# Performance work log

Measured on AMD Instinct MI355X. Metric: run time of the kernel, lower is better.

The kernel has to match this reference:

```python
import jax, jax.numpy as jnp
import numpy as np
from functools import partial

L, B, D_IN, D_MODEL, D_OUT, D_STATE = 2048, 8, 128, 256, 32, 16
D_INNER, DT_RANK, K_CONV = 2 * D_MODEL, D_MODEL // 16, 4
LOG2PI = float(np.log(2.0 * np.pi))


def setup_inputs() -> dict:
    key = jax.random.key(0)
    ks = jax.random.split(key, 16)
    sc = 0.02
    inp = {
        "s": jax.random.normal(ks[0], (L, B, D_IN), jnp.float32),
        "a": jax.random.normal(ks[1], (L, B, D_OUT), jnp.float32),
        # embedding linear
        "W_emb": jax.random.normal(ks[2], (D_IN, D_MODEL), jnp.float32) * sc,
        "b_emb": jnp.zeros((D_MODEL,), jnp.float32),
        # mamba block params
        "norm_w": jnp.ones((D_MODEL,), jnp.float32),
        "W_in": jax.random.normal(ks[3], (D_MODEL, 2 * D_INNER), jnp.float32) * sc,
        "conv_w": jax.random.normal(ks[4], (D_INNER, 1, K_CONV), jnp.float32) * sc,
        "conv_b": jnp.zeros((D_INNER,), jnp.float32),
        "W_x": jax.random.normal(ks[5], (D_INNER, DT_RANK + 2 * D_STATE), jnp.float32) * sc,
        "W_dt": jax.random.normal(ks[6], (DT_RANK, D_INNER), jnp.float32) * sc,
        "b_dt": jnp.full((D_INNER,), -2.0, jnp.float32),  # softplus(-2) ~ small init dt
        "A_log": jnp.broadcast_to(jnp.log(jnp.arange(1, D_STATE + 1, dtype=jnp.float32)), (D_INNER, D_STATE)).copy(),
        "D": jnp.ones((D_INNER,), jnp.float32),
        "W_out": jax.random.normal(ks[7], (D_INNER, D_MODEL), jnp.float32) * sc,
        # action head + log_std
        "W_head": jax.random.normal(ks[8], (D_MODEL, D_OUT), jnp.float32) * sc,
        "b_head": jnp.zeros((D_OUT,), jnp.float32),
        "log_std": jnp.zeros((D_OUT,), jnp.float32),
    }
    return inp


def _rmsnorm(x, w, eps=1e-5):
    return x * jax.lax.rsqrt(jnp.mean(x * x, axis=-1, keepdims=True) + eps) * w


def _silu(x):
    return x * jax.nn.sigmoid(x)


def _mamba_block(x, norm_w, W_in, conv_w, conv_b, W_x, W_dt, b_dt, A_log, D, W_out):
    # x: (B, L, d_model)
    resid = x
    xn = _rmsnorm(x, norm_w)
    xz = xn @ W_in                                  # (B, L, 2*d_inner)
    xp, z = jnp.split(xz, 2, axis=-1)
    # causal depthwise conv over time
    xc = jax.lax.conv_general_dilated(
        xp.transpose(0, 2, 1), conv_w, window_strides=(1,),
        padding=[(K_CONV - 1, 0)], feature_group_count=D_INNER,
        dimension_numbers=("NCH", "OIH", "NCH"))
    xp = _silu((xc + conv_b[None, :, None]).transpose(0, 2, 1))  # (B, L, d_inner)
    # input-dependent SSM params
    x_dbl = xp @ W_x                                # (B, L, dt_rank + 2*d_state)
    dt, Bm, Cm = jnp.split(x_dbl, [DT_RANK, DT_RANK + D_STATE], axis=-1)
    dt = jax.nn.softplus(dt @ W_dt + b_dt)          # (B, L, d_inner)
    A = -jnp.exp(A_log)                             # (d_inner, d_state)

    def step(h, t):
        dt_t, B_t, C_t, x_t = t                     # (B,d_i) (B,d_s) (B,d_s) (B,d_i)
        dA = jnp.exp(dt_t[..., None] * A)           # (B, d_inner, d_state)
        dBx = (dt_t * x_t)[..., None] * B_t[:, None, :]
        h = dA * h + dBx
        y = jnp.einsum("bds,bs->bd", h, C_t)
        return h, y

    h0 = jnp.zeros((x.shape[0], D_INNER, D_STATE), x.dtype)
    tm = lambda u: jnp.moveaxis(u, 1, 0)            # time-major
    _, ys = jax.lax.scan(step, h0, (tm(dt), tm(Bm), tm(Cm), tm(xp)))
    y = jnp.moveaxis(ys, 0, 1) + xp * D             # (B, L, d_inner)
    y = y * _silu(z)
    return y @ W_out + resid


def reference(s, a, W_emb, b_emb, norm_w, W_in, conv_w, conv_b, W_x, W_dt, b_dt,
              A_log, D, W_out, W_head, b_head, log_std):
    x = s @ W_emb + b_emb                           # (L, B, d_model)
    x = x.transpose(1, 0, 2)                        # (B, L, d_model)
    x = _mamba_block(x, norm_w, W_in, conv_w, conv_b, W_x, W_dt, b_dt, A_log, D, W_out)
    x = x.transpose(1, 0, 2)                        # (L, B, d_model)
    mu = x @ W_head + b_head                        # (L, B, d_out)
    # Normal(mu, exp(log_std)).log_prob(a).sum(-1)
    z = (a - mu) * jnp.exp(-log_std)
    logp = -0.5 * z * z - log_std - 0.5 * LOG2PI
    return logp.sum(axis=-1)                        # (L, B)
```

## Files before the change

kernel.cpp:

```cpp
#include <hip/hip_runtime.h>

typedef unsigned short u16;
typedef short bf16x8 __attribute__((ext_vector_type(8)));
typedef float floatx4 __attribute__((ext_vector_type(4)));

#define LSEQ 2048
#define BB 8
#define NTOK (LSEQ*BB)
#define DMODEL 256
#define DINNER 512
#define NSEG 128
#define SEGLEN 16

__device__ __forceinline__ float siluf(float x){ return x / (1.f + __expf(-x)); }
__device__ __forceinline__ float b2f(u16 x){ return __uint_as_float(((unsigned)x) << 16); }
__device__ __forceinline__ u16 f2b(float f){
  unsigned u = __float_as_uint(f);
  unsigned r = (u + 0x7fffu + ((u >> 16) & 1u)) >> 16;
  return (u16)r;
}

__global__ __launch_bounds__(256) void prep_k(
    const float* __restrict__ s, const float* __restrict__ Wemb,
    const float* __restrict__ Win, const float* __restrict__ Wout,
    const float* __restrict__ Wx, const float* __restrict__ Wdt,
    const float* __restrict__ Wh,
    u16* __restrict__ sb, u16* __restrict__ WTe, u16* __restrict__ WTi,
    u16* __restrict__ WTo, u16* __restrict__ WxT, u16* __restrict__ WdtTp,
    u16* __restrict__ WhT)
{
  int g = blockIdx.x, tid = threadIdx.x;
  if (g < 2048) {
    int i = (g*256 + tid)*4;
    float4 v = *(const float4*)&s[i];
    ushort4 o; o.x=f2b(v.x); o.y=f2b(v.y); o.z=f2b(v.z); o.w=f2b(v.w);
    *(ushort4*)&sb[i] = o;
  } else if (g < 2176) {
    int idx = (g-2048)*256 + tid; int n = idx >> 7, k = idx & 127;
    WTe[idx] = f2b(Wemb[(size_t)k*256 + n]);
  } else if (g < 3200) {
    int idx = (g-2176)*256 + tid; int n = idx >> 8, k = idx & 255;
    WTi[idx] = f2b(Win[(size_t)k*1024 + n]);
  } else if (g < 3712) {
    int idx = (g-3200)*256 + tid; int n = idx >> 9, k = idx & 511;
    WTo[idx] = f2b(Wout[(size_t)k*256 + n]);
  } else if (g < 3808) {
    int idx = (g-3712)*256 + tid; int n = idx >> 9, k = idx & 511;
    WxT[idx] = f2b(Wx[(size_t)k*48 + n]);
  } else if (g < 3872) {
    int idx = (g-3808)*256 + tid; int c = idx >> 5, r = idx & 31;
    WdtTp[idx] = (r < 16) ? f2b(Wdt[(size_t)r*512 + c]) : (u16)0;
  } else {
    int idx = (g-3872)*256 + tid; int j = idx >> 8, k = idx & 255;
    WhT[idx] = f2b(Wh[(size_t)k*32 + j]);
  }
}

template<int K, int OUTB>
__global__ __launch_bounds__(256) void gemm_mfma(
    const u16* __restrict__ Ab, const u16* __restrict__ WT,
    const float* __restrict__ bias, void* __restrict__ Cv, int N)
{
  __shared__ u16 SH[128*136];
  u16* As = SH;
  u16* Bs = SH + 128*40;
  const int tid = threadIdx.x;
  const int wave = tid >> 6, lane = tid & 63;
  const int quad = lane >> 4, l16 = lane & 15;
  const int bm0 = blockIdx.x*128, bn0 = blockIdx.y*128;
  const int wm = (wave & 1)*64, wn = (wave >> 1)*64;
  const int srow = tid >> 2, sch = (tid & 3)*8;
  floatx4 acc[4][4];
  #pragma unroll
  for (int r = 0; r < 4; ++r)
    #pragma unroll
    for (int c = 0; c < 4; ++c) acc[r][c] = (floatx4){0.f,0.f,0.f,0.f};

  for (int k0 = 0; k0 < K; k0 += 32) {
    #pragma unroll
    for (int p = 0; p < 2; ++p) {
      int row = srow + p*64;
      *(uint4*)&As[row*40 + sch] = *(const uint4*)&Ab[(size_t)(bm0+row)*K + k0 + sch];
      *(uint4*)&Bs[row*40 + sch] = *(const uint4*)&WT[(size_t)(bn0+row)*K + k0 + sch];
    }
    __syncthreads();
    bf16x8 af[4], bf[4];
    #pragma unroll
    for (int r = 0; r < 4; ++r) af[r] = *(const bf16x8*)&As[(wm + r*16 + l16)*40 + quad*8];
    #pragma unroll
    for (int c = 0; c < 4; ++c) bf[c] = *(const bf16x8*)&Bs[(wn + c*16 + l16)*40 + quad*8];
    #pragma unroll
    for (int r = 0; r < 4; ++r)
      #pragma unroll
      for (int c = 0; c < 4; ++c)
        acc[r][c] = __builtin_amdgcn_mfma_f32_16x16x32_bf16(af[r], bf[c], acc[r][c], 0, 0, 0);
    __syncthreads();
  }

  if (OUTB) {
    u16* Cs = SH;
    #pragma unroll
    for (int c = 0; c < 4; ++c) {
      int nl = wn + c*16 + l16;
      float bv = bias ? bias[bn0 + nl] : 0.f;
      #pragma unroll
      for (int r = 0; r < 4; ++r)
        #pragma unroll
        for (int reg = 0; reg < 4; ++reg) {
          int ml = wm + r*16 + quad*4 + reg;
          Cs[ml*136 + nl] = f2b(acc[r][c][reg] + bv);
        }
    }
    __syncthreads();
    #pragma unroll
    for (int p = 0; p < 8; ++p) {
      int row = p*16 + (tid >> 4);
      int col = (tid & 15)*8;
      uint4 v = *(const uint4*)&Cs[row*136 + col];
      *(uint4*)&((u16*)Cv)[(size_t)(bm0+row)*N + bn0 + col] = v;
    }
  } else {
    float* Cf = (float*)SH;
    #pragma unroll
    for (int half = 0; half < 2; ++half) {
      if ((wave & 1) == half) {
        #pragma unroll
        for (int c = 0; c < 4; ++c) {
          int nl = wn + c*16 + l16;
          float bv = bias ? bias[bn0 + nl] : 0.f;
          #pragma unroll
          for (int r = 0; r < 4; ++r)
            #pragma unroll
            for (int reg = 0; reg < 4; ++reg) {
              int ml = r*16 + quad*4 + reg;
              Cf[ml*132 + nl] = acc[r][c][reg] + bv;
            }
        }
      }
      __syncthreads();
      #pragma unroll
      for (int p = 0; p < 8; ++p) {
        int row = p*8 + (tid >> 5);
        int col = (tid & 31)*4;
        float4 v = *(const float4*)&Cf[row*132 + col];
        *(float4*)&((float*)Cv)[(size_t)(bm0 + half*64 + row)*N + bn0 + col] = v;
      }
      __syncthreads();
    }
  }
}

__global__ __launch_bounds__(256) void rmsnorm_k(const float* __restrict__ X,
    const float* __restrict__ w, u16* __restrict__ XNb)
{
  int n = blockIdx.x*4 + (threadIdx.x >> 6);
  int lane = threadIdx.x & 63;
  const float4 x = *(const float4*)&X[(size_t)n*DMODEL + lane*4];
  float ss = x.x*x.x + x.y*x.y + x.z*x.z + x.w*x.w;
  #pragma unroll
  for (int m = 1; m < 64; m <<= 1) ss += __shfl_xor(ss, m);
  float r = rsqrtf(ss * (1.f/DMODEL) + 1e-5f);
  ushort4 o;
  o.x = f2b(x.x * r * w[lane*4+0]);
  o.y = f2b(x.y * r * w[lane*4+1]);
  o.z = f2b(x.z * r * w[lane*4+2]);
  o.w = f2b(x.w * r * w[lane*4+3]);
  *(ushort4*)&XNb[(size_t)n*DMODEL + lane*4] = o;
}

__global__ __launch_bounds__(256) void conv_silu_k(const u16* __restrict__ XZb,
    const float* __restrict__ cw, const float* __restrict__ cb,
    u16* __restrict__ XPb)
{
  int g = blockIdx.x*256 + threadIdx.x;
  int c4 = (g & 127) << 2;
  int n = g >> 7;
  int l = n >> 3;
  float w[4][4];
  #pragma unroll
  for (int i = 0; i < 4; ++i)
    #pragma unroll
    for (int k = 0; k < 4; ++k) w[i][k] = cw[(c4+i)*4 + k];
  float acc[4];
  #pragma unroll
  for (int i = 0; i < 4; ++i) acc[i] = cb[c4+i];
  #pragma unroll
  for (int k = 0; k < 4; ++k) {
    int lp = l - 3 + k;
    if (lp >= 0) {
      const ushort4 xv = *(const ushort4*)&XZb[(size_t)(n - BB*(3-k))*1024 + c4];
      acc[0] = fmaf(w[0][k], b2f(xv.x), acc[0]);
      acc[1] = fmaf(w[1][k], b2f(xv.y), acc[1]);
      acc[2] = fmaf(w[2][k], b2f(xv.z), acc[2]);
      acc[3] = fmaf(w[3][k], b2f(xv.w), acc[3]);
    }
  }
  ushort4 ob;
  ob.x = f2b(siluf(acc[0])); ob.y = f2b(siluf(acc[1]));
  ob.z = f2b(siluf(acc[2])); ob.w = f2b(siluf(acc[3]));
  *(ushort4*)&XPb[(size_t)n*DINNER + c4] = ob;
}

__global__ __launch_bounds__(128) void xdblBC_k(const u16* __restrict__ XPb,
    const u16* __restrict__ WxT,
    float* __restrict__ BM, float* __restrict__ CM, u16* __restrict__ DTRb)
{
  const int tid = threadIdx.x;
  const int wave = tid >> 6, lane = tid & 63;
  const int quad = lane >> 4, l16 = lane & 15;
  const int tok0 = blockIdx.x*32 + wave*16;

  floatx4 acc[3];
  #pragma unroll
  for (int j = 0; j < 3; ++j) acc[j] = (floatx4){0.f,0.f,0.f,0.f};
  const u16* Ap = XPb + (size_t)(tok0 + l16)*DINNER + quad*8;
  const u16* Bp = WxT + (size_t)l16*DINNER + quad*8;
  #pragma unroll
  for (int k0 = 0; k0 < DINNER; k0 += 32) {
    bf16x8 af = *(const bf16x8*)(Ap + k0);
    #pragma unroll
    for (int j = 0; j < 3; ++j) {
      bf16x8 bf = *(const bf16x8*)(Bp + (size_t)j*16*DINNER + k0);
      acc[j] = __builtin_amdgcn_mfma_f32_16x16x32_bf16(af, bf, acc[j], 0, 0, 0);
    }
  }
  #pragma unroll
  for (int reg = 0; reg < 4; ++reg) {
    size_t t = (size_t)(tok0 + quad*4 + reg);
    BM[t*16 + l16] = acc[1][reg];
    CM[t*16 + l16] = acc[2][reg];
    DTRb[t*32 + l16]      = f2b(acc[0][reg]);
    DTRb[t*32 + 16 + l16] = 0;
  }
}

__global__ __launch_bounds__(256) void dtg_k(const u16* __restrict__ DTRb,
    const u16* __restrict__ WdtTp, const float* __restrict__ bdt,
    u16* __restrict__ DTb)
{
  __shared__ u16 Cs[128*136];
  const int tid = threadIdx.x;
  const int wave = tid >> 6, lane = tid & 63;
  const int quad = lane >> 4, l16 = lane & 15;
  const int bm0 = blockIdx.x*128, bn0 = blockIdx.y*128;
  const int bm = bm0 + (wave & 1)*64;
  const int bn = bn0 + (wave >> 1)*64;
  bf16x8 af[4], bf[4];
  #pragma unroll
  for (int r = 0; r < 4; ++r)
    af[r] = *(const bf16x8*)(DTRb + (size_t)(bm + r*16 + l16)*32 + quad*8);
  #pragma unroll
  for (int c = 0; c < 4; ++c)
    bf[c] = *(const bf16x8*)(WdtTp + (size_t)(bn + c*16 + l16)*32 + quad*8);
  #pragma unroll
  for (int c = 0; c < 4; ++c) {
    int nl = (wave >> 1)*64 + c*16 + l16;
    float bd = bdt[bn0 + nl];
    #pragma unroll
    for (int r = 0; r < 4; ++r) {
      floatx4 d = __builtin_amdgcn_mfma_f32_16x16x32_bf16(af[r], bf[c],
                    (floatx4){0.f,0.f,0.f,0.f}, 0, 0, 0);
      #pragma unroll
      for (int reg = 0; reg < 4; ++reg) {
        int ml = (wave & 1)*64 + r*16 + quad*4 + reg;
        float sum = d[reg] + bd;
        Cs[ml*136 + nl] = f2b((sum > 20.f) ? sum : __logf(1.f + __expf(sum)));
      }
    }
  }
  __syncthreads();
  #pragma unroll
  for (int p = 0; p < 8; ++p) {
    int row = p*16 + (tid >> 4);
    int col = (tid & 15)*8;
    uint4 v = *(const uint4*)&Cs[row*136 + col];
    *(uint4*)&DTb[(size_t)(bm0+row)*DINNER + bn0 + col] = v;
  }
}

__global__ __launch_bounds__(256) void scanA_k(const u16* __restrict__ DTb,
    const u16* __restrict__ XPb, const float* __restrict__ BM,
    const float* __restrict__ Alog, u16* __restrict__ HENDb, float* __restrict__ DTS)
{
  __shared__ __align__(16) float Bs[SEGLEN*16];
  const int tid = threadIdx.x;
  const int seg = blockIdx.x, b = blockIdx.y, half = blockIdx.z;
  const int c = half*256 + tid;
  const int t0 = seg*SEGLEN;
  {
    int t = tid >> 4, s = tid & 15;
    Bs[tid] = BM[((size_t)(t0+t)*BB + b)*16 + s];
  }
  float As[16];
  #pragma unroll
  for (int s = 0; s < 16; ++s) As[s] = -__expf(Alog[c*16+s]);
  bool uni = true;
  #pragma unroll
  for (int s = 1; s < 16; ++s)
    uni = uni && (fabsf(As[s] - As[0]*(float)(s+1)) <= 1e-4f*(float)(s+1));
  float h[16];
  #pragma unroll
  for (int s = 0; s < 16; ++s) h[s] = 0.f;
  float dts = 0.f;
  __syncthreads();
  const size_t base = (size_t)t0*BB + b;
  const u16* dtp = DTb + base*DINNER + c;
  const u16* xpp = XPb + base*DINNER + c;
  float dt = b2f(dtp[0]);
  float xp = b2f(xpp[0]);
  for (int t = 0; t < SEGLEN; ++t) {
    float dtn = 0.f, xpn = 0.f;
    if (t+1 < SEGLEN) {
      dtn = b2f(dtp[(size_t)(t+1)*BB*DINNER]);
      xpn = b2f(xpp[(size_t)(t+1)*BB*DINNER]);
    }
    dts += dt;
    float dtx = dt * xp;
    const float4 b0 = *(const float4*)&Bs[t*16+0];
    const float4 b1 = *(const float4*)&Bs[t*16+4];
    const float4 b2 = *(const float4*)&Bs[t*16+8];
    const float4 b3 = *(const float4*)&Bs[t*16+12];
    const float bv[16] = {b0.x,b0.y,b0.z,b0.w, b1.x,b1.y,b1.z,b1.w,
                          b2.x,b2.y,b2.z,b2.w, b3.x,b3.y,b3.z,b3.w};
    float dA[16];
    if (uni) {
      float p = __expf(dt*As[0]);
      dA[0] = p;
      #pragma unroll
      for (int s = 1; s < 16; ++s) dA[s] = dA[s-1]*p;
    } else {
      #pragma unroll
      for (int s = 0; s < 16; ++s) dA[s] = __expf(dt*As[s]);
    }
    #pragma unroll
    for (int s = 0; s < 16; ++s)
      h[s] = fmaf(dA[s], h[s], dtx*bv[s]);
    dt = dtn; xp = xpn;
  }
  u16* hp = &HENDb[(((size_t)seg*BB + b)*DINNER + c)*16];
  #pragma unroll
  for (int q = 0; q < 2; ++q) {
    ushort4 v0, v1;
    v0.x = f2b(h[q*8+0]); v0.y = f2b(h[q*8+1]); v0.z = f2b(h[q*8+2]); v0.w = f2b(h[q*8+3]);
    v1.x = f2b(h[q*8+4]); v1.y = f2b(h[q*8+5]); v1.z = f2b(h[q*8+6]); v1.w = f2b(h[q*8+7]);
    *(ushort4*)&hp[q*8]     = v0;
    *(ushort4*)&hp[q*8 + 4] = v1;
  }
  DTS[((size_t)seg*BB + b)*DINNER + c] = dts;
}

__global__ __launch_bounds__(256) void stitch_k(u16* __restrict__ HENDb,
    const float* __restrict__ DTS, const float* __restrict__ Alog)
{
  int g = blockIdx.x*256 + threadIdx.x;
  int b = g >> 13;
  int rem = g & 8191;
  int cidx = rem >> 4;
  float A = -__expf(Alog[rem]);
  float h0 = 0.f;
  for (int k = 0; k < NSEG; ++k) {
    size_t idx = (((size_t)k*BB + b) << 13) + rem;
    float hend = b2f(HENDb[idx]);
    HENDb[idx] = f2b(h0);
    float dts = DTS[((size_t)k*BB + b)*DINNER + cidx];
    h0 = fmaf(__expf(dts*A), h0, hend);
  }
}

__global__ __launch_bounds__(256) void scanC_k(const u16* __restrict__ DTb,
    const u16* __restrict__ XPb, const float* __restrict__ BM, const float* __restrict__ CM,
    const u16* __restrict__ XZb, const float* __restrict__ Alog, const float* __restrict__ Dp,
    const u16* __restrict__ H0b, u16* __restrict__ YGb)
{
  __shared__ __align__(16) float Bs[SEGLEN*16];
  __shared__ __align__(16) float Cs[SEGLEN*16];
  const int tid = threadIdx.x;
  const int seg = blockIdx.x, b = blockIdx.y, half = blockIdx.z;
  const int c = half*256 + tid;
  const int t0 = seg*SEGLEN;
  {
    int t = tid >> 4, s = tid & 15;
    size_t nb = ((size_t)(t0+t)*BB + b)*16 + s;
    Bs[tid] = BM[nb];
    Cs[tid] = CM[nb];
  }
  float As[16];
  #pragma unroll
  for (int s = 0; s < 16; ++s) As[s] = -__expf(Alog[c*16+s]);
  bool uni = true;
  #pragma unroll
  for (int s = 1; s < 16; ++s)
    uni = uni && (fabsf(As[s] - As[0]*(float)(s+1)) <= 1e-4f*(float)(s+1));
  float h[16];
  const u16* hp = &H0b[(((size_t)seg*BB + b)*DINNER + c)*16];
  #pragma unroll
  for (int q = 0; q < 4; ++q) {
    ushort4 hv = *(const ushort4*)&hp[q*4];
    h[q*4+0]=b2f(hv.x); h[q*4+1]=b2f(hv.y); h[q*4+2]=b2f(hv.z); h[q*4+3]=b2f(hv.w);
  }
  const float Dv = Dp[c];
  __syncthreads();
  const size_t base = (size_t)t0*BB + b;
  const u16* dtp = DTb + base*DINNER + c;
  const u16* xpp = XPb + base*DINNER + c;
  const u16* zp  = XZb + base*1024 + DINNER + c;
  u16*       ygp = YGb + base*DINNER + c;
  float dt = b2f(dtp[0]);
  float xp = b2f(xpp[0]);
  float zg = b2f(zp[0]);
  for (int t = 0; t < SEGLEN; ++t) {
    float dtn = 0.f, xpn = 0.f, zgn = 0.f;
    if (t+1 < SEGLEN) {
      dtn = b2f(dtp[(size_t)(t+1)*BB*DINNER]);
      xpn = b2f(xpp[(size_t)(t+1)*BB*DINNER]);
      zgn = b2f(zp[(size_t)(t+1)*BB*1024]);
    }
    float dtx = dt * xp;
    const float4 b0 = *(const float4*)&Bs[t*16+0];
    const float4 b1 = *(const float4*)&Bs[t*16+4];
    const float4 b2 = *(const float4*)&Bs[t*16+8];
    const float4 b3 = *(const float4*)&Bs[t*16+12];
    const float4 c0 = *(const float4*)&Cs[t*16+0];
    const float4 c1 = *(const float4*)&Cs[t*16+4];
    const float4 c2 = *(const float4*)&Cs[t*16+8];
    const float4 c3 = *(const float4*)&Cs[t*16+12];
    const float bv[16] = {b0.x,b0.y,b0.z,b0.w, b1.x,b1.y,b1.z,b1.w,
                          b2.x,b2.y,b2.z,b2.w, b3.x,b3.y,b3.z,b3.w};
    const float cv[16] = {c0.x,c0.y,c0.z,c0.w, c1.x,c1.y,c1.z,c1.w,
                          c2.x,c2.y,c2.z,c2.w, c3.x,c3.y,c3.z,c3.w};
    float dA[16];
    if (uni) {
      float p = __expf(dt*As[0]);
      dA[0] = p;
      #pragma unroll
      for (int s = 1; s < 16; ++s) dA[s] = dA[s-1]*p;
    } else {
      #pragma unroll
      for (int s = 0; s < 16; ++s) dA[s] = __expf(dt*As[s]);
    }
    float y0 = 0.f, y1 = 0.f, y2 = 0.f, y3 = 0.f;
    #pragma unroll
    for (int q = 0; q < 4; ++q) {
      h[q*4+0] = fmaf(dA[q*4+0], h[q*4+0], dtx*bv[q*4+0]);
      h[q*4+1] = fmaf(dA[q*4+1], h[q*4+1], dtx*bv[q*4+1]);
      h[q*4+2] = fmaf(dA[q*4+2], h[q*4+2], dtx*bv[q*4+2]);
      h[q*4+3] = fmaf(dA[q*4+3], h[q*4+3], dtx*bv[q*4+3]);
      y0 = fmaf(h[q*4+0], cv[q*4+0], y0);
      y1 = fmaf(h[q*4+1], cv[q*4+1], y1);
      y2 = fmaf(h[q*4+2], cv[q*4+2], y2);
      y3 = fmaf(h[q*4+3], cv[q*4+3], y3);
    }
    float y = (y0+y1) + (y2+y3);
    ygp[(size_t)t*BB*DINNER] = f2b((y + xp*Dv) * siluf(zg));
    dt = dtn; xp = xpn; zg = zgn;
  }
}

__global__ __launch_bounds__(256) void outhead_k(const u16* __restrict__ YGb,
    const u16* __restrict__ WTo, const float* __restrict__ Xres,
    const u16* __restrict__ WhT, const float* __restrict__ bh,
    const float* __restrict__ lstd, const float* __restrict__ a,
    float* __restrict__ out)
{
  __shared__ u16 Xs[64*264];
  u16* As = Xs;
  u16* Bs = Xs + 64*40;
  const int tid = threadIdx.x;
  const int wave = tid >> 6, lane = tid & 63;
  const int quad = lane >> 4, l16 = lane & 15;
  const int m0 = blockIdx.x*64;
  const int n0 = wave*64;
  const int srow = tid >> 2, sch = (tid & 3)*8;
  floatx4 acc[4][4];
  #pragma unroll
  for (int r = 0; r < 4; ++r)
    #pragma unroll
    for (int c = 0; c < 4; ++c) acc[r][c] = (floatx4){0.f,0.f,0.f,0.f};

  for (int k0 = 0; k0 < DINNER; k0 += 32) {
    if (srow < 64)
      *(uint4*)&As[srow*40 + sch] = *(const uint4*)&YGb[(size_t)(m0+srow)*DINNER + k0 + sch];
    #pragma unroll
    for (int p = 0; p < 4; ++p) {
      int row = srow + p*64;
      *(uint4*)&Bs[row*40 + sch] = *(const uint4*)&WTo[(size_t)row*DINNER + k0 + sch];
    }
    __syncthreads();
    bf16x8 af[4], bf[4];
    #pragma unroll
    for (int r = 0; r < 4; ++r) af[r] = *(const bf16x8*)&As[(r*16 + l16)*40 + quad*8];
    #pragma unroll
    for (int c = 0; c < 4; ++c) bf[c] = *(const bf16x8*)&Bs[(n0 + c*16 + l16)*40 + quad*8];
    #pragma unroll
    for (int r = 0; r < 4; ++r)
      #pragma unroll
      for (int c = 0; c < 4; ++c)
        acc[r][c] = __builtin_amdgcn_mfma_f32_16x16x32_bf16(af[r], bf[c], acc[r][c], 0, 0, 0);
    __syncthreads();
  }
  #pragma unroll
  for (int c = 0; c < 4; ++c) {
    int n = n0 + c*16 + l16;
    #pragma unroll
    for (int r = 0; r < 4; ++r) {
      #pragma unroll
      for (int reg = 0; reg < 4; ++reg) {
        int ml = r*16 + quad*4 + reg;
        float t = acc[r][c][reg] + Xres[(size_t)(m0 + ml)*DMODEL + n];
        Xs[ml*264 + n] = f2b(t);
      }
    }
  }
  __syncthreads();
  floatx4 mu[2];
  mu[0] = (floatx4){0.f,0.f,0.f,0.f};
  mu[1] = (floatx4){0.f,0.f,0.f,0.f};
  #pragma unroll
  for (int k0 = 0; k0 < DMODEL; k0 += 32) {
    bf16x8 axf = *(const bf16x8*)&Xs[(wave*16 + l16)*264 + k0 + quad*8];
    #pragma unroll
    for (int nt = 0; nt < 2; ++nt) {
      bf16x8 bwf = *(const bf16x8*)(WhT + (size_t)(nt*16 + l16)*DMODEL + k0 + quad*8);
      mu[nt] = __builtin_amdgcn_mfma_f32_16x16x32_bf16(axf, bwf, mu[nt], 0, 0, 0);
    }
  }
  float ls0 = lstd[l16],      els0 = __expf(-ls0), bh0 = bh[l16];
  float ls1 = lstd[16 + l16], els1 = __expf(-ls1), bh1 = bh[16 + l16];
  #pragma unroll
  for (int reg = 0; reg < 4; ++reg) {
    int tok = m0 + wave*16 + quad*4 + reg;
    float m0v = mu[0][reg] + bh0;
    float m1v = mu[1][reg] + bh1;
    float z0 = (a[(size_t)tok*32 + l16]      - m0v) * els0;
    float z1 = (a[(size_t)tok*32 + 16 + l16] - m1v) * els1;
    float t = (-0.5f*z0*z0 - ls0) + (-0.5f*z1*z1 - ls1) - 2.f*0.91893853320467274f;
    t += __shfl_xor(t, 1);
    t += __shfl_xor(t, 2);
    t += __shfl_xor(t, 4);
    t += __shfl_xor(t, 8);
    if (l16 == 0) out[tok] = t;
  }
}

extern "C" void kernel_launch(void* const* d_in, const int* in_sizes, int n_in,
                              void* d_out, int out_size, void* d_ws, size_t ws_size,
                              hipStream_t stream)
{
  const float* s    = (const float*)d_in[0];
  const float* a    = (const float*)d_in[1];
  const float* Wemb = (const float*)d_in[2];
  const float* bemb = (const float*)d_in[3];
  const float* nw   = (const float*)d_in[4];
  const float* Win  = (const float*)d_in[5];
  const float* cw   = (const float*)d_in[6];
  const float* cb   = (const float*)d_in[7];
  const float* Wx   = (const float*)d_in[8];
  const float* Wdt  = (const float*)d_in[9];
  const float* bdt  = (const float*)d_in[10];
  const float* Alog = (const float*)d_in[11];
  const float* Dp   = (const float*)d_in[12];
  const float* Wout = (const float*)d_in[13];
  const float* Wh   = (const float*)d_in[14];
  const float* bh   = (const float*)d_in[15];
  const float* lstd = (const float*)d_in[16];

  float* X    = (float*)d_ws;
  u16*   XZb  = (u16*)(X + (size_t)NTOK*DMODEL);
  u16*   XPb  = XZb + (size_t)NTOK*1024;
  u16*   DTb  = XPb + (size_t)NTOK*DINNER;
  u16*   YGb  = DTb + (size_t)NTOK*DINNER;
  u16*   sb   = YGb + (size_t)NTOK*DINNER;
  u16*   XNb  = sb  + (size_t)NTOK*128;
  u16*   WTe  = XNb + (size_t)NTOK*DMODEL;
  u16*   WTi  = WTe + 256*128;
  u16*   WTo  = WTi + 1024*256;
  u16*   WxT  = WTo + 256*512;
  u16*   WdtTp= WxT + 48*512;
  u16*   WhT  = WdtTp + 512*32;
  u16*   DTRb = WhT + 32*256;
  u16*   HENDb= DTRb + (size_t)NTOK*32;
  float* BM   = (float*)(HENDb + (size_t)NSEG*BB*DINNER*16);
  float* CM   = BM + (size_t)NTOK*16;
  float* DTS  = CM + (size_t)NTOK*16;
  float* out  = (float*)d_out;

  prep_k          <<<3904,        256, 0, stream>>>(s, Wemb, Win, Wout, Wx, Wdt, Wh,
                                                    sb, WTe, WTi, WTo, WxT, WdtTp, WhT);
  gemm_mfma<128,0><<<dim3(128,2), 256, 0, stream>>>(sb,  WTe, bemb,   X,   DMODEL);
  rmsnorm_k       <<<4096,        256, 0, stream>>>(X, nw, XNb);
  gemm_mfma<256,1><<<dim3(128,8), 256, 0, stream>>>(XNb, WTi, nullptr, XZb, 1024);
  conv_silu_k     <<<8192,        256, 0, stream>>>(XZb, cw, cb, XPb);
  xdblBC_k        <<<512,         128, 0, stream>>>(XPb, WxT, BM, CM, DTRb);
  dtg_k           <<<dim3(128,4), 256, 0, stream>>>(DTRb, WdtTp, bdt, DTb);
  scanA_k         <<<dim3(NSEG,BB,2), 256, 0, stream>>>(DTb, XPb, BM, Alog, HENDb, DTS);
  stitch_k        <<<256,         256, 0, stream>>>(HENDb, DTS, Alog);
  scanC_k         <<<dim3(NSEG,BB,2), 256, 0, stream>>>(DTb, XPb, BM, CM, XZb, Alog, Dp, HENDb, YGb);
  outhead_k       <<<256,         256, 0, stream>>>(YGb, WTo, X, WhT, bh, lstd, a, out);
}
```

Measured before the change: 252.4 us.

## Fuse embedding with RMSNorm, fold conv+SiLU into consumers, store residual as bf16

Merges the s conversion, embedding GEMM and RMSNorm into one kernel that writes a bf16 residual and the normalized activations. Removes the standalone conv_silu kernel and its XP buffer: the causal conv and SiLU are recomputed inside the x_dbl GEMM tile loader and inside both scan kernels from XZ. The residual becomes bf16 instead of fp32, which cuts memory traffic and launches but adds redundant conv work and some rounding of the residual.

```diff
diff --git a/kernel.cpp b/kernel.cpp
--- a/kernel.cpp
+++ b/kernel.cpp
@@ -21,45 +21,138 @@
 }
 
 __global__ __launch_bounds__(256) void prep_k(
-    const float* __restrict__ s, const float* __restrict__ Wemb,
-    const float* __restrict__ Win, const float* __restrict__ Wout,
-    const float* __restrict__ Wx, const float* __restrict__ Wdt,
-    const float* __restrict__ Wh,
-    u16* __restrict__ sb, u16* __restrict__ WTe, u16* __restrict__ WTi,
-    u16* __restrict__ WTo, u16* __restrict__ WxT, u16* __restrict__ WdtTp,
-    u16* __restrict__ WhT)
+    const float* __restrict__ Wemb, const float* __restrict__ Win,
+    const float* __restrict__ Wout, const float* __restrict__ Wx,
+    const float* __restrict__ Wdt, const float* __restrict__ Wh,
+    u16* __restrict__ WTe, u16* __restrict__ WTi, u16* __restrict__ WTo,
+    u16* __restrict__ WxT, u16* __restrict__ WdtTp, u16* __restrict__ WhT)
 {
   int g = blockIdx.x, tid = threadIdx.x;
-  if (g < 2048) {
-    int i = (g*256 + tid)*4;
-    float4 v = *(const float4*)&s[i];
-    ushort4 o; o.x=f2b(v.x); o.y=f2b(v.y); o.z=f2b(v.z); o.w=f2b(v.w);
-    *(ushort4*)&sb[i] = o;
-  } else if (g < 2176) {
-    int idx = (g-2048)*256 + tid; int n = idx >> 7, k = idx & 127;
+  if (g < 128) {
+    int idx = g*256 + tid; int n = idx >> 7, k = idx & 127;
     WTe[idx] = f2b(Wemb[(size_t)k*256 + n]);
-  } else if (g < 3200) {
-    int idx = (g-2176)*256 + tid; int n = idx >> 8, k = idx & 255;
+  } else if (g < 1152) {
+    int idx = (g-128)*256 + tid; int n = idx >> 8, k = idx & 255;
     WTi[idx] = f2b(Win[(size_t)k*1024 + n]);
-  } else if (g < 3712) {
-    int idx = (g-3200)*256 + tid; int n = idx >> 9, k = idx & 511;
+  } else if (g < 1664) {
+    int idx = (g-1152)*256 + tid; int n = idx >> 9, k = idx & 511;
     WTo[idx] = f2b(Wout[(size_t)k*256 + n]);
-  } else if (g < 3808) {
-    int idx = (g-3712)*256 + tid; int n = idx >> 9, k = idx & 511;
+  } else if (g < 1760) {
+    int idx = (g-1664)*256 + tid; int n = idx >> 9, k = idx & 511;
     WxT[idx] = f2b(Wx[(size_t)k*48 + n]);
-  } else if (g < 3872) {
-    int idx = (g-3808)*256 + tid; int c = idx >> 5, r = idx & 31;
+  } else if (g < 1824) {
+    int idx = (g-1760)*256 + tid; int c = idx >> 5, r = idx & 31;
     WdtTp[idx] = (r < 16) ? f2b(Wdt[(size_t)r*512 + c]) : (u16)0;
   } else {
-    int idx = (g-3872)*256 + tid; int j = idx >> 8, k = idx & 255;
+    int idx = (g-1824)*256 + tid; int j = idx >> 8, k = idx & 255;
     WhT[idx] = f2b(Wh[(size_t)k*32 + j]);
   }
 }
 
-template<int K, int OUTB>
+__global__ __launch_bounds__(256) void embnorm_k(
+    const float* __restrict__ s, const u16* __restrict__ WTe,
+    const float* __restrict__ bemb, const float* __restrict__ nw,
+    u16* __restrict__ Xb, u16* __restrict__ XNb)
+{
+  __shared__ u16 SH[64*264];
+  __shared__ float ssq[64*4];
+  __shared__ float rr[64];
+  u16* As = SH;
+  u16* Bs = SH + 64*40;
+  const int tid = threadIdx.x;
+  const int wave = tid >> 6, lane = tid & 63;
+  const int quad = lane >> 4, l16 = lane & 15;
+  const int m0 = blockIdx.x*64;
+  const int wn = wave*64;
+  const int srow = tid >> 2, sch = (tid & 3)*8;
+  floatx4 acc[4][4];
+  #pragma unroll
+  for (int r = 0; r < 4; ++r)
+    #pragma unroll
+    for (int c = 0; c < 4; ++c) acc[r][c] = (floatx4){0.f,0.f,0.f,0.f};
+
+  for (int k0 = 0; k0 < 128; k0 += 32) {
+    {
+      float4 v0 = *(const float4*)&s[(size_t)(m0+srow)*128 + k0 + sch];
+      float4 v1 = *(const float4*)&s[(size_t)(m0+srow)*128 + k0 + sch + 4];
+      __align__(16) u16 o[8];
+      o[0]=f2b(v0.x); o[1]=f2b(v0.y); o[2]=f2b(v0.z); o[3]=f2b(v0.w);
+      o[4]=f2b(v1.x); o[5]=f2b(v1.y); o[6]=f2b(v1.z); o[7]=f2b(v1.w);
+      *(uint4*)&As[srow*40 + sch] = *(const uint4*)o;
+    }
+    #pragma unroll
+    for (int p = 0; p < 4; ++p) {
+      int row = srow + p*64;
+      *(uint4*)&Bs[row*40 + sch] = *(const uint4*)&WTe[(size_t)row*128 + k0 + sch];
+    }
+    __syncthreads();
+    bf16x8 af[4], bf[4];
+    #pragma unroll
+    for (int r = 0; r < 4; ++r) af[r] = *(const bf16x8*)&As[(r*16 + l16)*40 + quad*8];
+    #pragma unroll
+    for (int c = 0; c < 4; ++c) bf[c] = *(const bf16x8*)&Bs[(wn + c*16 + l16)*40 + quad*8];
+    #pragma unroll
+    for (int r = 0; r < 4; ++r)
+      #pragma unroll
+      for (int c = 0; c < 4; ++c)
+        acc[r][c] = __builtin_amdgcn_mfma_f32_16x16x32_bf16(af[r], bf[c], acc[r][c], 0, 0, 0);
+    __syncthreads();
+  }
+  u16* Xs = SH;
+  #pragma unroll
+  for (int c = 0; c < 4; ++c) {
+    int n = wn + c*16 + l16;
+    float bv = bemb[n];
+    #pragma unroll
+    for (int r = 0; r < 4; ++r)
+      #pragma unroll
+      for (int reg = 0; reg < 4; ++reg) {
+        int ml = r*16 + quad*4 + reg;
+        Xs[ml*264 + n] = f2b(acc[r][c][reg] + bv);
+      }
+  }
+  __syncthreads();
+  #pragma unroll
+  for (int p = 0; p < 8; ++p) {
+    int row = p*8 + (tid >> 5);
+    int col = (tid & 31)*8;
+    *(uint4*)&Xb[(size_t)(m0+row)*256 + col] = *(const uint4*)&Xs[row*264 + col];
+  }
+  const int tk = tid >> 2, q = tid & 3;
+  float ss = 0.f;
+  #pragma unroll
+  for (int j = 0; j < 8; ++j) {
+    uint4 v = *(const uint4*)&Xs[tk*264 + q*64 + j*8];
+    const u16* u = (const u16*)&v;
+    #pragma unroll
+    for (int i = 0; i < 8; ++i) { float x = b2f(u[i]); ss += x*x; }
+  }
+  ssq[tk*4 + q] = ss;
+  __syncthreads();
+  if (q == 0)
+    rr[tk] = rsqrtf((ssq[tk*4]+ssq[tk*4+1]+ssq[tk*4+2]+ssq[tk*4+3])*(1.f/DMODEL) + 1e-5f);
+  __syncthreads();
+  float r = rr[tk];
+  #pragma unroll
+  for (int j = 0; j < 8; ++j) {
+    int idx = q*64 + j*8;
+    uint4 v = *(const uint4*)&Xs[tk*264 + idx];
+    const u16* u = (const u16*)&v;
+    float4 w0 = *(const float4*)&nw[idx];
+    float4 w1 = *(const float4*)&nw[idx+4];
+    __align__(16) u16 o[8];
+    o[0]=f2b(b2f(u[0])*r*w0.x); o[1]=f2b(b2f(u[1])*r*w0.y);
+    o[2]=f2b(b2f(u[2])*r*w0.z); o[3]=f2b(b2f(u[3])*r*w0.w);
+    o[4]=f2b(b2f(u[4])*r*w1.x); o[5]=f2b(b2f(u[5])*r*w1.y);
+    o[6]=f2b(b2f(u[6])*r*w1.z); o[7]=f2b(b2f(u[7])*r*w1.w);
+    *(uint4*)&XNb[(size_t)(m0+tk)*256 + idx] = *(const uint4*)o;
+  }
+}
+
+template<int K>
 __global__ __launch_bounds__(256) void gemm_mfma(
     const u16* __restrict__ Ab, const u16* __restrict__ WT,
-    const float* __restrict__ bias, void* __restrict__ Cv, int N)
+    u16* __restrict__ Cv, int N)
 {
   __shared__ u16 SH[128*136];
   u16* As = SH;
@@ -96,134 +189,80 @@
         acc[r][c] = __builtin_amdgcn_mfma_f32_16x16x32_bf16(af[r], bf[c], acc[r][c], 0, 0, 0);
     __syncthreads();
   }
-
-  if (OUTB) {
-    u16* Cs = SH;
-    #pragma unroll
-    for (int c = 0; c < 4; ++c) {
-      int nl = wn + c*16 + l16;
-      float bv = bias ? bias[bn0 + nl] : 0.f;
-      #pragma unroll
-      for (int r = 0; r < 4; ++r)
-        #pragma unroll
-        for (int reg = 0; reg < 4; ++reg) {
-          int ml = wm + r*16 + quad*4 + reg;
-          Cs[ml*136 + nl] = f2b(acc[r][c][reg] + bv);
-        }
-    }
-    __syncthreads();
-    #pragma unroll
-    for (int p = 0; p < 8; ++p) {
-      int row = p*16 + (tid >> 4);
-      int col = (tid & 15)*8;
-      uint4 v = *(const uint4*)&Cs[row*136 + col];
-      *(uint4*)&((u16*)Cv)[(size_t)(bm0+row)*N + bn0 + col] = v;
-    }
-  } else {
-    float* Cf = (float*)SH;
-    #pragma unroll
-    for (int half = 0; half < 2; ++half) {
-      if ((wave & 1) == half) {
-        #pragma unroll
-        for (int c = 0; c < 4; ++c) {
-          int nl = wn + c*16 + l16;
-          float bv = bias ? bias[bn0 + nl] : 0.f;
-          #pragma unroll
-          for (int r = 0; r < 4; ++r)
-            #pragma unroll
-            for (int reg = 0; reg < 4; ++reg) {
-              int ml = r*16 + quad*4 + reg;
-              Cf[ml*132 + nl] = acc[r][c][reg] + bv;
-            }
-        }
+  u16* Cs = SH;
+  #pragma unroll
+  for (int c = 0; c < 4; ++c) {
+    int nl = wn + c*16 + l16;
+    #pragma unroll
+    for (int r = 0; r < 4; ++r)
+      #pragma unroll
+      for (int reg = 0; reg < 4; ++reg) {
+        int ml = wm + r*16 + quad*4 + reg;
+        Cs[ml*136 + nl] = f2b(acc[r][c][reg]);
       }
-      __syncthreads();
-      #pragma unroll
-      for (int p = 0; p < 8; ++p) {
-        int row = p*8 + (tid >> 5);
-        int col = (tid & 31)*4;
-        float4 v = *(const float4*)&Cf[row*132 + col];
-        *(float4*)&((float*)Cv)[(size_t)(bm0 + half*64 + row)*N + bn0 + col] = v;
-      }
-      __syncthreads();
-    }
-  }
-}
-
-__global__ __launch_bounds__(256) void rmsnorm_k(const float* __restrict__ X,
-    const float* __restrict__ w, u16* __restrict__ XNb)
-{
-  int n = blockIdx.x*4 + (threadIdx.x >> 6);
-  int lane = threadIdx.x & 63;
-  const float4 x = *(const float4*)&X[(size_t)n*DMODEL + lane*4];
-  float ss = x.x*x.x + x.y*x.y + x.z*x.z + x.w*x.w;
-  #pragma unroll
-  for (int m = 1; m < 64; m <<= 1) ss += __shfl_xor(ss, m);
-  float r = rsqrtf(ss * (1.f/DMODEL) + 1e-5f);
-  ushort4 o;
-  o.x = f2b(x.x * r * w[lane*4+0]);
-  o.y = f2b(x.y * r * w[lane*4+1]);
-  o.z = f2b(x.z * r * w[lane*4+2]);
-  o.w = f2b(x.w * r * w[lane*4+3]);
-  *(ushort4*)&XNb[(size_t)n*DMODEL + lane*4] = o;
-}
-
-__global__ __launch_bounds__(256) void conv_silu_k(const u16* __restrict__ XZb,
+  }
+  __syncthreads();
+  #pragma unroll
+  for (int p = 0; p < 8; ++p) {
+    int row = p*16 + (tid >> 4);
+    int col = (tid & 15)*8;
+    uint4 v = *(const uint4*)&Cs[row*136 + col];
+    *(uint4*)&Cv[(size_t)(bm0+row)*N + bn0 + col] = v;
+  }
+}
+
+__global__ __launch_bounds__(256) void xdblBC_k(const u16* __restrict__ XZb,
     const float* __restrict__ cw, const float* __restrict__ cb,
-    u16* __restrict__ XPb)
-{
-  int g = blockIdx.x*256 + threadIdx.x;
-  int c4 = (g & 127) << 2;
-  int n = g >> 7;
-  int l = n >> 3;
-  float w[4][4];
-  #pragma unroll
-  for (int i = 0; i < 4; ++i)
-    #pragma unroll
-    for (int k = 0; k < 4; ++k) w[i][k] = cw[(c4+i)*4 + k];
-  float acc[4];
-  #pragma unroll
-  for (int i = 0; i < 4; ++i) acc[i] = cb[c4+i];
-  #pragma unroll
-  for (int k = 0; k < 4; ++k) {
-    int lp = l - 3 + k;
-    if (lp >= 0) {
-      const ushort4 xv = *(const ushort4*)&XZb[(size_t)(n - BB*(3-k))*1024 + c4];
-      acc[0] = fmaf(w[0][k], b2f(xv.x), acc[0]);
-      acc[1] = fmaf(w[1][k], b2f(xv.y), acc[1]);
-      acc[2] = fmaf(w[2][k], b2f(xv.z), acc[2]);
-      acc[3] = fmaf(w[3][k], b2f(xv.w), acc[3]);
-    }
-  }
-  ushort4 ob;
-  ob.x = f2b(siluf(acc[0])); ob.y = f2b(siluf(acc[1]));
-  ob.z = f2b(siluf(acc[2])); ob.w = f2b(siluf(acc[3]));
-  *(ushort4*)&XPb[(size_t)n*DINNER + c4] = ob;
-}
-
-__global__ __launch_bounds__(128) void xdblBC_k(const u16* __restrict__ XPb,
     const u16* __restrict__ WxT,
     float* __restrict__ BM, float* __restrict__ CM, u16* __restrict__ DTRb)
 {
+  __shared__ u16 As[64*40];
+  __shared__ u16 Ws[48*40];
+  __shared__ float CWs[512*4];
+  __shared__ float CBs[512];
   const int tid = threadIdx.x;
   const int wave = tid >> 6, lane = tid & 63;
   const int quad = lane >> 4, l16 = lane & 15;
-  const int tok0 = blockIdx.x*32 + wave*16;
-
+  const int m0 = blockIdx.x*64;
+  const int srow = tid >> 2, sch = (tid & 3)*8;
+  const int n = m0 + srow;
+  for (int e = tid; e < 2048; e += 256) CWs[e] = cw[e];
+  for (int e = tid; e < 512;  e += 256) CBs[e] = cb[e];
   floatx4 acc[3];
   #pragma unroll
   for (int j = 0; j < 3; ++j) acc[j] = (floatx4){0.f,0.f,0.f,0.f};
-  const u16* Ap = XPb + (size_t)(tok0 + l16)*DINNER + quad*8;
-  const u16* Bp = WxT + (size_t)l16*DINNER + quad*8;
-  #pragma unroll
+  __syncthreads();
+  const bf16x8 z8 = {0,0,0,0,0,0,0,0};
   for (int k0 = 0; k0 < DINNER; k0 += 32) {
-    bf16x8 af = *(const bf16x8*)(Ap + k0);
+    bf16x8 t3 = *(const bf16x8*)&XZb[(size_t)n*1024 + k0 + sch];
+    bf16x8 t2 = z8, t1 = z8, t0v = z8;
+    if (n >= 8)  t2  = *(const bf16x8*)&XZb[(size_t)(n-8)*1024  + k0 + sch];
+    if (n >= 16) t1  = *(const bf16x8*)&XZb[(size_t)(n-16)*1024 + k0 + sch];
+    if (n >= 24) t0v = *(const bf16x8*)&XZb[(size_t)(n-24)*1024 + k0 + sch];
+    __align__(16) u16 outa[8];
+    #pragma unroll
+    for (int j = 0; j < 8; ++j) {
+      int c = k0 + sch + j;
+      float4 wv = *(const float4*)&CWs[c*4];
+      float xc = CBs[c] + wv.x*b2f((u16)t0v[j]) + wv.y*b2f((u16)t1[j])
+               + wv.z*b2f((u16)t2[j]) + wv.w*b2f((u16)t3[j]);
+      outa[j] = f2b(siluf(xc));
+    }
+    *(uint4*)&As[srow*40 + sch] = *(const uint4*)outa;
+    if (tid < 192) {
+      int wr = tid >> 2;
+      *(uint4*)&Ws[wr*40 + sch] = *(const uint4*)&WxT[(size_t)wr*512 + k0 + sch];
+    }
+    __syncthreads();
+    bf16x8 af = *(const bf16x8*)&As[(wave*16 + l16)*40 + quad*8];
     #pragma unroll
     for (int j = 0; j < 3; ++j) {
-      bf16x8 bf = *(const bf16x8*)(Bp + (size_t)j*16*DINNER + k0);
+      bf16x8 bf = *(const bf16x8*)&Ws[(j*16 + l16)*40 + quad*8];
       acc[j] = __builtin_amdgcn_mfma_f32_16x16x32_bf16(af, bf, acc[j], 0, 0, 0);
     }
-  }
+    __syncthreads();
+  }
+  const int tok0 = m0 + wave*16;
   #pragma unroll
   for (int reg = 0; reg < 4; ++reg) {
     size_t t = (size_t)(tok0 + quad*4 + reg);
@@ -279,7 +318,8 @@
 }
 
 __global__ __launch_bounds__(256) void scanA_k(const u16* __restrict__ DTb,
-    const u16* __restrict__ XPb, const float* __restrict__ BM,
+    const u16* __restrict__ XZb, const float* __restrict__ BM,
+    const float* __restrict__ cw, const float* __restrict__ cb,
     const float* __restrict__ Alog, u16* __restrict__ HENDb, float* __restrict__ DTS)
 {
   __shared__ __align__(16) float Bs[SEGLEN*16];
@@ -298,6 +338,8 @@
   #pragma unroll
   for (int s = 1; s < 16; ++s)
     uni = uni && (fabsf(As[s] - As[0]*(float)(s+1)) <= 1e-4f*(float)(s+1));
+  const float4 cwv = *(const float4*)&cw[c*4];
+  const float cbv = cb[c];
   float h[16];
   #pragma unroll
   for (int s = 0; s < 16; ++s) h[s] = 0.f;
@@ -305,15 +347,20 @@
   __syncthreads();
   const size_t base = (size_t)t0*BB + b;
   const u16* dtp = DTb + base*DINNER + c;
-  const u16* xpp = XPb + base*DINNER + c;
+  const u16* xzp = XZb + base*1024 + c;
+  float w0 = (t0 >= 3) ? b2f(xzp[-(size_t)3*BB*1024]) : 0.f;
+  float w1 = (t0 >= 2) ? b2f(xzp[-(size_t)2*BB*1024]) : 0.f;
+  float w2 = (t0 >= 1) ? b2f(xzp[-(size_t)1*BB*1024]) : 0.f;
   float dt = b2f(dtp[0]);
-  float xp = b2f(xpp[0]);
+  float xz = b2f(xzp[0]);
   for (int t = 0; t < SEGLEN; ++t) {
-    float dtn = 0.f, xpn = 0.f;
+    float dtn = 0.f, xzn = 0.f;
     if (t+1 < SEGLEN) {
       dtn = b2f(dtp[(size_t)(t+1)*BB*DINNER]);
-      xpn = b2f(xpp[(size_t)(t+1)*BB*DINNER]);
-    }
+      xzn = b2f(xzp[(size_t)(t+1)*BB*1024]);
+    }
+    float xp = siluf(cbv + cwv.x*w0 + cwv.y*w1 + cwv.z*w2 + cwv.w*xz);
+    w0 = w1; w1 = w2; w2 = xz;
     dts += dt;
     float dtx = dt * xp;
     const float4 b0 = *(const float4*)&Bs[t*16+0];
@@ -335,7 +382,7 @@
     #pragma unroll
     for (int s = 0; s < 16; ++s)
       h[s] = fmaf(dA[s], h[s], dtx*bv[s]);
-    dt = dtn; xp = xpn;
+    dt = dtn; xz = xzn;
   }
   u16* hp = &HENDb[(((size_t)seg*BB + b)*DINNER + c)*16];
   #pragma unroll
@@ -368,8 +415,9 @@
 }
 
 __global__ __launch_bounds__(256) void scanC_k(const u16* __restrict__ DTb,
-    const u16* __restrict__ XPb, const float* __restrict__ BM, const float* __restrict__ CM,
-    const u16* __restrict__ XZb, const float* __restrict__ Alog, const float* __restrict__ Dp,
+    const u16* __restrict__ XZb, const float* __restrict__ BM, const float* __restrict__ CM,
+    const float* __restrict__ cw, const float* __restrict__ cb,
+    const float* __restrict__ Alog, const float* __restrict__ Dp,
     const u16* __restrict__ H0b, u16* __restrict__ YGb)
 {
   __shared__ __align__(16) float Bs[SEGLEN*16];
@@ -391,6 +439,8 @@
   #pragma unroll
   for (int s = 1; s < 16; ++s)
     uni = uni && (fabsf(As[s] - As[0]*(float)(s+1)) <= 1e-4f*(float)(s+1));
+  const float4 cwv = *(const float4*)&cw[c*4];
+  const float cbv = cb[c];
   float h[16];
   const u16* hp = &H0b[(((size_t)seg*BB + b)*DINNER + c)*16];
   #pragma unroll
@@ -402,19 +452,24 @@
   __syncthreads();
   const size_t base = (size_t)t0*BB + b;
   const u16* dtp = DTb + base*DINNER + c;
-  const u16* xpp = XPb + base*DINNER + c;
+  const u16* xzp = XZb + base*1024 + c;
   const u16* zp  = XZb + base*1024 + DINNER + c;
   u16*       ygp = YGb + base*DINNER + c;
+  float w0 = (t0 >= 3) ? b2f(xzp[-(size_t)3*BB*1024]) : 0.f;
+  float w1 = (t0 >= 2) ? b2f(xzp[-(size_t)2*BB*1024]) : 0.f;
+  float w2 = (t0 >= 1) ? b2f(xzp[-(size_t)1*BB*1024]) : 0.f;
   float dt = b2f(dtp[0]);
-  float xp = b2f(xpp[0]);
+  float xz = b2f(xzp[0]);
   float zg = b2f(zp[0]);
   for (int t = 0; t < SEGLEN; ++t) {
-    float dtn = 0.f, xpn = 0.f, zgn = 0.f;
+    float dtn = 0.f, xzn = 0.f, zgn = 0.f;
     if (t+1 < SEGLEN) {
       dtn = b2f(dtp[(size_t)(t+1)*BB*DINNER]);
-      xpn = b2f(xpp[(size_t)(t+1)*BB*DINNER]);
+      xzn = b2f(xzp[(size_t)(t+1)*BB*1024]);
       zgn = b2f(zp[(size_t)(t+1)*BB*1024]);
     }
+    float xp = siluf(cbv + cwv.x*w0 + cwv.y*w1 + cwv.z*w2 + cwv.w*xz);
+    w0 = w1; w1 = w2; w2 = xz;
     float dtx = dt * xp;
     const float4 b0 = *(const float4*)&Bs[t*16+0];
     const float4 b1 = *(const float4*)&Bs[t*16+4];
@@ -424,10 +479,10 @@
     const float4 c1 = *(const float4*)&Cs[t*16+4];
     const float4 c2 = *(const float4*)&Cs[t*16+8];
     const float4 c3 = *(const float4*)&Cs[t*16+12];
-    const float bv[16] = {b0.x,b0.y,b0.z,b0.w, b1.x,b1.y,b1.z,b1.w,
-                          b2.x,b2.y,b2.z,b2.w, b3.x,b3.y,b3.z,b3.w};
-    const float cv[16] = {c0.x,c0.y,c0.z,c0.w, c1.x,c1.y,c1.z,c1.w,
-                          c2.x,c2.y,c2.z,c2.w, c3.x,c3.y,c3.z,c3.w};
+    const float bvv[16] = {b0.x,b0.y,b0.z,b0.w, b1.x,b1.y,b1.z,b1.w,
+                           b2.x,b2.y,b2.z,b2.w, b3.x,b3.y,b3.z,b3.w};
+    const float cvv[16] = {c0.x,c0.y,c0.z,c0.w, c1.x,c1.y,c1.z,c1.w,
+                           c2.x,c2.y,c2.z,c2.w, c3.x,c3.y,c3.z,c3.w};
     float dA[16];
     if (uni) {
       float p = __expf(dt*As[0]);
@@ -441,23 +496,23 @@
     float y0 = 0.f, y1 = 0.f, y2 = 0.f, y3 = 0.f;
     #pragma unroll
     for (int q = 0; q < 4; ++q) {
-      h[q*4+0] = fmaf(dA[q*4+0], h[q*4+0], dtx*bv[q*4+0]);
-      h[q*4+1] = fmaf(dA[q*4+1], h[q*4+1], dtx*bv[q*4+1]);
-      h[q*4+2] = fmaf(dA[q*4+2], h[q*4+2], dtx*bv[q*4+2]);
-      h[q*4+3] = fmaf(dA[q*4+3], h[q*4+3], dtx*bv[q*4+3]);
-      y0 = fmaf(h[q*4+0], cv[q*4+0], y0);
-      y1 = fmaf(h[q*4+1], cv[q*4+1], y1);
-      y2 = fmaf(h[q*4+2], cv[q*4+2], y2);
-      y3 = fmaf(h[q*4+3], cv[q*4+3], y3);
+      h[q*4+0] = fmaf(dA[q*4+0], h[q*4+0], dtx*bvv[q*4+0]);
+      h[q*4+1] = fmaf(dA[q*4+1], h[q*4+1], dtx*bvv[q*4+1]);
+      h[q*4+2] = fmaf(dA[q*4+2], h[q*4+2], dtx*bvv[q*4+2]);
+      h[q*4+3] = fmaf(dA[q*4+3], h[q*4+3], dtx*bvv[q*4+3]);
+      y0 = fmaf(h[q*4+0], cvv[q*4+0], y0);
+      y1 = fmaf(h[q*4+1], cvv[q*4+1], y1);
+      y2 = fmaf(h[q*4+2], cvv[q*4+2], y2);
+      y3 = fmaf(h[q*4+3], cvv[q*4+3], y3);
     }
     float y = (y0+y1) + (y2+y3);
     ygp[(size_t)t*BB*DINNER] = f2b((y + xp*Dv) * siluf(zg));
-    dt = dtn; xp = xpn; zg = zgn;
+    dt = dtn; xz = xzn; zg = zgn;
   }
 }
 
 __global__ __launch_bounds__(256) void outhead_k(const u16* __restrict__ YGb,
-    const u16* __restrict__ WTo, const float* __restrict__ Xres,
+    const u16* __restrict__ WTo, const u16* __restrict__ Xb,
     const u16* __restrict__ WhT, const float* __restrict__ bh,
     const float* __restrict__ lstd, const float* __restrict__ a,
     float* __restrict__ out)
@@ -499,6 +554,13 @@
     __syncthreads();
   }
   #pragma unroll
+  for (int p = 0; p < 8; ++p) {
+    int row = p*8 + (tid >> 5);
+    int col = (tid & 31)*8;
+    *(uint4*)&Xs[row*264 + col] = *(const uint4*)&Xb[(size_t)(m0+row)*256 + col];
+  }
+  __syncthreads();
+  #pragma unroll
   for (int c = 0; c < 4; ++c) {
     int n = n0 + c*16 + l16;
     #pragma unroll
@@ -506,8 +568,7 @@
       #pragma unroll
       for (int reg = 0; reg < 4; ++reg) {
         int ml = r*16 + quad*4 + reg;
-        float t = acc[r][c][reg] + Xres[(size_t)(m0 + ml)*DMODEL + n];
-        Xs[ml*264 + n] = f2b(t);
+        Xs[ml*264 + n] = f2b(acc[r][c][reg] + b2f(Xs[ml*264 + n]));
       }
     }
   }
@@ -564,14 +625,12 @@
   const float* bh   = (const float*)d_in[15];
   const float* lstd = (const float*)d_in[16];
 
-  float* X    = (float*)d_ws;
-  u16*   XZb  = (u16*)(X + (size_t)NTOK*DMODEL);
-  u16*   XPb  = XZb + (size_t)NTOK*1024;
-  u16*   DTb  = XPb + (size_t)NTOK*DINNER;
+  u16*   Xb   = (u16*)d_ws;
+  u16*   XZb  = Xb  + (size_t)NTOK*DMODEL;
+  u16*   XNb  = XZb + (size_t)NTOK*1024;
+  u16*   DTb  = XNb + (size_t)NTOK*DMODEL;
   u16*   YGb  = DTb + (size_t)NTOK*DINNER;
-  u16*   sb   = YGb + (size_t)NTOK*DINNER;
-  u16*   XNb  = sb  + (size_t)NTOK*128;
-  u16*   WTe  = XNb + (size_t)NTOK*DMODEL;
+  u16*   WTe  = YGb + (size_t)NTOK*DINNER;
   u16*   WTi  = WTe + 256*128;
   u16*   WTo  = WTi + 1024*256;
   u16*   WxT  = WTo + 256*512;
@@ -584,16 +643,14 @@
   float* DTS  = CM + (size_t)NTOK*16;
   float* out  = (float*)d_out;
 
-  prep_k          <<<3904,        256, 0, stream>>>(s, Wemb, Win, Wout, Wx, Wdt, Wh,
-                                                    sb, WTe, WTi, WTo, WxT, WdtTp, WhT);
-  gemm_mfma<128,0><<<dim3(128,2), 256, 0, stream>>>(sb,  WTe, bemb,   X,   DMODEL);
-  rmsnorm_k       <<<4096,        256, 0, stream>>>(X, nw, XNb);
-  gemm_mfma<256,1><<<dim3(128,8), 256, 0, stream>>>(XNb, WTi, nullptr, XZb, 1024);
-  conv_silu_k     <<<8192,        256, 0, stream>>>(XZb, cw, cb, XPb);
-  xdblBC_k        <<<512,         128, 0, stream>>>(XPb, WxT, BM, CM, DTRb);
-  dtg_k           <<<dim3(128,4), 256, 0, stream>>>(DTRb, WdtTp, bdt, DTb);
-  scanA_k         <<<dim3(NSEG,BB,2), 256, 0, stream>>>(DTb, XPb, BM, Alog, HENDb, DTS);
-  stitch_k        <<<256,         256, 0, stream>>>(HENDb, DTS, Alog);
-  scanC_k         <<<dim3(NSEG,BB,2), 256, 0, stream>>>(DTb, XPb, BM, CM, XZb, Alog, Dp, HENDb, YGb);
-  outhead_k       <<<256,         256, 0, stream>>>(YGb, WTo, X, WhT, bh, lstd, a, out);
-}
+  prep_k       <<<1856,        256, 0, stream>>>(Wemb, Win, Wout, Wx, Wdt, Wh,
+                                                 WTe, WTi, WTo, WxT, WdtTp, WhT);
+  embnorm_k    <<<256,         256, 0, stream>>>(s, WTe, bemb, nw, Xb, XNb);
+  gemm_mfma<256><<<dim3(128,8), 256, 0, stream>>>(XNb, WTi, XZb, 1024);
+  xdblBC_k     <<<256,         256, 0, stream>>>(XZb, cw, cb, WxT, BM, CM, DTRb);
+  dtg_k        <<<dim3(128,4), 256, 0, stream>>>(DTRb, WdtTp, bdt, DTb);
+  scanA_k      <<<dim3(NSEG,BB,2), 256, 0, stream>>>(DTb, XZb, BM, cw, cb, Alog, HENDb, DTS);
+  stitch_k     <<<256,         256, 0, stream>>>(HENDb, DTS, Alog);
+  scanC_k      <<<dim3(NSEG,BB,2), 256, 0, stream>>>(DTb, XZb, BM, CM, cw, cb, Alog, Dp, HENDb, YGb);
+  outhead_k    <<<256,         256, 0, stream>>>(YGb, WTo, Xb, WhT, bh, lstd, a, out);
+}
```

New measurement: 247.8 us. About the same (-1.8%).
